# Kernel optimization log

Measured on AMD Instinct MI355X. Metric: run time of the kernel, lower is better.

The kernel has to match this reference:

```python
import jax, jax.numpy as jnp
import numpy as np

B, KEY, D, U, MODES = 16384, 64, 128, 128, 32

def setup_inputs() -> dict:
    key = jax.random.key(0)
    k1, k2, k3, k4, k5 = jax.random.split(key, 5)
    return {
        "key": jax.random.normal(k1, (B, KEY), dtype=jnp.float32),
        "x": jax.random.normal(k2, (B, D), dtype=jnp.float32),
        "sens": jnp.ones((MODES,), dtype=jnp.float32),
        "keys_map": jax.random.normal(k3, (MODES, KEY), dtype=jnp.float32),
        "kernels": jax.random.normal(k4, (MODES, D, U), dtype=jnp.float32) * 0.05,
        "biases": jax.random.normal(k5, (MODES, U), dtype=jnp.float32) * 0.05,
    }

def reference(key, x, sens, keys_map, kernels, biases):
    # key: [B, KEY]; keys_map: [MODES, KEY]
    # Euclidean distance of each key to each mode's stored key.
    dist = jnp.sqrt(jnp.sum((key[:, None, :] - keys_map[None, :, :]) ** 2, axis=-1))  # [B, MODES]
    sim = jax.nn.softmax(sens / (dist + 1.0), axis=-1)  # [B, MODES]
    modes = kernels.shape[0]
    # Original: kernel_b = mean_m(sim[b,m] * kernels[m]); out_b = x_b @ kernel_b.
    # Reordered as GEMM-per-mode + weighted combine (same math):
    out = jnp.einsum('bm,bd,mdu->bu', sim, x, kernels) / modes  # [B, U]
    out = out + (sim @ biases) / modes  # mean over modes of sim-weighted biases
    return out
```

## Files before the change

### kernel.cpp

```cpp
#include <hip/hip_runtime.h>

#define BATCH 16384
#define KEYD  64
#define DDIM  128
#define UDIM  128
#define MODES 32

typedef __attribute__((ext_vector_type(8))) short bf16x8;
typedef __attribute__((ext_vector_type(4))) float f32x4;

__device__ __forceinline__ unsigned short f2bf(float f) {
  unsigned u = __float_as_uint(f);
  unsigned r = (u + 0x7FFFu + ((u >> 16) & 1u)) >> 16;
  return (unsigned short)r;
}

__device__ __forceinline__ void gld_lds16(const void* g, void* l) {
  __builtin_amdgcn_global_load_lds(
      (const __attribute__((address_space(1))) unsigned int*)g,
      (__attribute__((address_space(3))) unsigned int*)l, 16, 0, 0);
}

__global__ __launch_bounds__(256) void prep_all(
    const float* __restrict__ key, const float* __restrict__ x,
    const float* __restrict__ sens, const float* __restrict__ keys_map,
    const float* __restrict__ kernels, const float* __restrict__ biases,
    float* __restrict__ sim, unsigned short* __restrict__ x16,
    unsigned short* __restrict__ kb16, unsigned short* __restrict__ bb16) {
  const int t = threadIdx.x;
  const int bid = blockIdx.x;

  if (bid < BATCH / 32) {
    __shared__ float kr[32][KEYD];
    *(float4*)(&kr[0][0] + t * 4) =
        *(const float4*)(key + (long)bid * 32 * KEYD + t * 4);
    *(float4*)(&kr[0][0] + 1024 + t * 4) =
        *(const float4*)(key + (long)bid * 32 * KEYD + 1024 + t * 4);

    const int lane = t & 63, wave = t >> 6;
    const int m = lane & 31, h = lane >> 5;
    float kreg[32];
    {
      const float* kmp = keys_map + m * KEYD + h * 32;
      #pragma unroll
      for (int j = 0; j < 32; j += 4) {
        const float4 v = *(const float4*)(kmp + j);
        kreg[j] = v.x; kreg[j + 1] = v.y; kreg[j + 2] = v.z; kreg[j + 3] = v.w;
      }
    }
    const float sv = sens[m];
    __syncthreads();

    #pragma unroll
    for (int rr = 0; rr < 8; ++rr) {
      const int rl = wave * 8 + rr;
      const long row = (long)bid * 32 + rl;

      float d2h = 0.f;
      #pragma unroll
      for (int j = 0; j < 32; j += 2) {
        const float2 kv = *(const float2*)(&kr[rl][h * 32 + j]);
        float a = kv.x - kreg[j], b = kv.y - kreg[j + 1];
        d2h += a * a + b * b;
      }
      float d2 = d2h + __shfl_xor(d2h, 32, 64);
      float logit = sv / (sqrtf(d2) + 1.0f);
      float mx = logit;
      #pragma unroll
      for (int off = 16; off > 0; off >>= 1) mx = fmaxf(mx, __shfl_xor(mx, off, 64));
      float e = __expf(logit - mx);
      float s = e;
      #pragma unroll
      for (int off = 16; off > 0; off >>= 1) s += __shfl_xor(s, off, 64);
      if (h == 0) sim[row * MODES + m] = e / s;

      const float2 xv = *(const float2*)(x + row * DDIM + lane * 2);
      ushort2 o; o.x = f2bf(xv.x); o.y = f2bf(xv.y);
      *(ushort2*)(x16 + row * DDIM + lane * 2) = o;
    }
  } else {
    int tt = (bid - BATCH / 32) * 256 + t;
    if (tt < MODES * 16 * UDIM) {
      int u = tt & 127, kb = (tt >> 7) & 15, m = tt >> 11;
      const float* src = kernels + (long)((m * 16 + kb) * 8) * UDIM + u;
      ushort4 lo, hi;
      lo.x = f2bf(src[0 * UDIM]); lo.y = f2bf(src[1 * UDIM]);
      lo.z = f2bf(src[2 * UDIM]); lo.w = f2bf(src[3 * UDIM]);
      hi.x = f2bf(src[4 * UDIM]); hi.y = f2bf(src[5 * UDIM]);
      hi.z = f2bf(src[6 * UDIM]); hi.w = f2bf(src[7 * UDIM]);
      *(ushort4*)(kb16 + (long)tt * 8) = lo;
      *(ushort4*)(kb16 + (long)tt * 8 + 4) = hi;
    } else {
      int tb = tt - MODES * 16 * UDIM;
      int u = tb & 127, kb = tb >> 7;
      const float* src = biases + kb * 8 * UDIM + u;
      ushort4 lo, hi;
      lo.x = f2bf(src[0 * UDIM]); lo.y = f2bf(src[1 * UDIM]);
      lo.z = f2bf(src[2 * UDIM]); lo.w = f2bf(src[3 * UDIM]);
      hi.x = f2bf(src[4 * UDIM]); hi.y = f2bf(src[5 * UDIM]);
      hi.z = f2bf(src[6 * UDIM]); hi.w = f2bf(src[7 * UDIM]);
      *(ushort4*)(bb16 + (long)tb * 8) = lo;
      *(ushort4*)(bb16 + (long)tb * 8 + 4) = hi;
    }
  }
}

#define MODE_STRIDE (16 * UDIM * 8)
#define HALF_STRIDE (16 * 64 * 8)

__global__ __launch_bounds__(256, 2) void gemm_fused(
    const unsigned short* __restrict__ x16, const unsigned short* __restrict__ kb16,
    const unsigned short* __restrict__ bb16, const float* __restrict__ sim,
    float* __restrict__ out) {
  __shared__ alignas(16) unsigned short bsh[2][2 * HALF_STRIDE];
  __shared__ float simT[MODES][64];

  const int t = threadIdx.x;
  const int lane = t & 63, w = t >> 6;
  const int q = lane >> 4, l16 = lane & 15;
  const long bm = (long)blockIdx.x * 64;
  const int ch = blockIdx.y;
  const int uc = w * 16 + l16;

  {
    const int r = t >> 2, mg = (t & 3) * 8;
    const float4 v0 = *(const float4*)(sim + (bm + r) * MODES + mg);
    const float4 v1 = *(const float4*)(sim + (bm + r) * MODES + mg + 4);
    simT[mg + 0][r] = v0.x; simT[mg + 1][r] = v0.y;
    simT[mg + 2][r] = v0.z; simT[mg + 3][r] = v0.w;
    simT[mg + 4][r] = v1.x; simT[mg + 5][r] = v1.y;
    simT[mg + 6][r] = v1.z; simT[mg + 7][r] = v1.w;
  }

  bf16x8 aF[4][4];
  #pragma unroll
  for (int rt = 0; rt < 4; ++rt)
    #pragma unroll
    for (int ks = 0; ks < 4; ++ks)
      aF[rt][ks] = *(const bf16x8*)(x16 + (bm + rt * 16 + l16) * DDIM + ks * 32 + q * 8);

  #pragma unroll
  for (int i = 0; i < 8; ++i) {
    const int c = i * 4 + w, ml = c >> 4, kb = c & 15;
    gld_lds16(kb16 + (long)ml * MODE_STRIDE + kb * (UDIM * 8) + ch * (64 * 8) + lane * 8,
              &bsh[0][(c * 64 + lane) * 8]);
  }

  f32x4 acc[4] = {};

  for (int s = 0; s < MODES / 2; ++s) {
    __syncthreads();
    if (s < MODES / 2 - 1) {
      const unsigned short* srcb = kb16 + (long)(s + 1) * 2 * MODE_STRIDE;
      unsigned short* dst = bsh[(s + 1) & 1];
      #pragma unroll
      for (int i = 0; i < 8; ++i) {
        const int c = i * 4 + w, ml = c >> 4, kb = c & 15;
        gld_lds16(srcb + (long)ml * MODE_STRIDE + kb * (UDIM * 8) + ch * (64 * 8) + lane * 8,
                  dst + (c * 64 + lane) * 8);
      }
    }

    const unsigned short* bs = bsh[s & 1];
    #pragma unroll
    for (int ml = 0; ml < 2; ++ml) {
      const int mi = s * 2 + ml;
      bf16x8 bF[4];
      #pragma unroll
      for (int ks = 0; ks < 4; ++ks)
        bF[ks] = *(const bf16x8*)&bs[ml * HALF_STRIDE + (((ks * 4 + q) * 64) + uc) * 8];

      f32x4 tmp[4] = {};
      #pragma unroll
      for (int ks = 0; ks < 4; ++ks)
        #pragma unroll
        for (int rt = 0; rt < 4; ++rt)
          tmp[rt] = __builtin_amdgcn_mfma_f32_16x16x32_bf16(aF[rt][ks], bF[ks], tmp[rt], 0, 0, 0);

      #pragma unroll
      for (int rt = 0; rt < 4; ++rt) {
        const f32x4 sv = *(const f32x4*)&simT[mi][rt * 16 + q * 4];
        acc[rt] += sv * tmp[rt];
      }
    }
  }

  {
    const bf16x8 bb = *(const bf16x8*)(bb16 + ((long)q * UDIM + ch * 64 + uc) * 8);
    #pragma unroll
    for (int rt = 0; rt < 4; ++rt) {
      const float* sp = sim + (bm + rt * 16 + l16) * MODES + q * 8;
      const float4 sv0 = *(const float4*)(sp);
      const float4 sv1 = *(const float4*)(sp + 4);
      bf16x8 sF;
      sF[0] = (short)f2bf(sv0.x); sF[1] = (short)f2bf(sv0.y);
      sF[2] = (short)f2bf(sv0.z); sF[3] = (short)f2bf(sv0.w);
      sF[4] = (short)f2bf(sv1.x); sF[5] = (short)f2bf(sv1.y);
      sF[6] = (short)f2bf(sv1.z); sF[7] = (short)f2bf(sv1.w);
      acc[rt] = __builtin_amdgcn_mfma_f32_16x16x32_bf16(sF, bb, acc[rt], 0, 0, 0);
    }
  }

  #pragma unroll
  for (int rt = 0; rt < 4; ++rt) {
    const long row = bm + rt * 16 + q * 4;
    #pragma unroll
    for (int r = 0; r < 4; ++r)
      out[(row + r) * UDIM + ch * 64 + uc] = acc[rt][r] * (1.0f / MODES);
  }
}

extern "C" void kernel_launch(void* const* d_in, const int* in_sizes, int n_in,
                              void* d_out, int out_size, void* d_ws, size_t ws_size,
                              hipStream_t stream) {
  const float* key      = (const float*)d_in[0];
  const float* x        = (const float*)d_in[1];
  const float* sens     = (const float*)d_in[2];
  const float* keys_map = (const float*)d_in[3];
  const float* kernels  = (const float*)d_in[4];
  const float* biases   = (const float*)d_in[5];
  float* out = (float*)d_out;

  char* ws = (char*)d_ws;
  float*          sim  = (float*)ws;
  unsigned short* x16  = (unsigned short*)(ws + (2u << 20));
  unsigned short* kb16 = (unsigned short*)(ws + (6u << 20));
  unsigned short* bb16 = (unsigned short*)(ws + (7u << 20));

  prep_all<<<BATCH / 32 + 258, 256, 0, stream>>>(
      key, x, sens, keys_map, kernels, biases, sim, x16, kb16, bb16);
  gemm_fused<<<dim3(BATCH / 64, 2), 256, 0, stream>>>(x16, kb16, bb16, sim, out);
}
```

Measured before the change: 107.9 us.

## Use per-wave private LDS staging with 4-deep vmcnt pipeline and remapped grid

```diff
diff --git a/kernel.cpp b/kernel.cpp
--- a/kernel.cpp
+++ b/kernel.cpp
@@ -106,20 +106,24 @@
 }
 
 #define MODE_STRIDE (16 * UDIM * 8)
-#define HALF_STRIDE (16 * 64 * 8)
+
+#define WAITV(n) asm volatile("s_waitcnt vmcnt(" #n ")" ::: "memory")
 
 __global__ __launch_bounds__(256, 2) void gemm_fused(
     const unsigned short* __restrict__ x16, const unsigned short* __restrict__ kb16,
     const unsigned short* __restrict__ bb16, const float* __restrict__ sim,
     float* __restrict__ out) {
-  __shared__ alignas(16) unsigned short bsh[2][2 * HALF_STRIDE];
+  __shared__ alignas(16) unsigned short bsh[4][4][2048];
   __shared__ float simT[MODES][64];
 
   const int t = threadIdx.x;
   const int lane = t & 63, w = t >> 6;
   const int q = lane >> 4, l16 = lane & 15;
-  const long bm = (long)blockIdx.x * 64;
-  const int ch = blockIdx.y;
+
+  const int bid0 = blockIdx.x;
+  const int lgc = (bid0 & 7) * 64 + (bid0 >> 3);
+  const int bx = lgc >> 1, ch = lgc & 1;
+  const long bm = (long)bx * 64;
   const int uc = w * 16 + l16;
 
   {
@@ -131,6 +135,7 @@
     simT[mg + 4][r] = v1.x; simT[mg + 5][r] = v1.y;
     simT[mg + 6][r] = v1.z; simT[mg + 7][r] = v1.w;
   }
+  __syncthreads();
 
   bf16x8 aF[4][4];
   #pragma unroll
@@ -139,51 +144,47 @@
     for (int ks = 0; ks < 4; ++ks)
       aF[rt][ks] = *(const bf16x8*)(x16 + (bm + rt * 16 + l16) * DDIM + ks * 32 + q * 8);
 
+  const int stg_g = ((lane >> 4) * UDIM + ch * 64 + w * 16 + (lane & 15)) * 8;
+
+#define STAGE(m, p) do {                                                        \
+    const unsigned short* sg = kb16 + (long)(m) * MODE_STRIDE + stg_g;          \
+    _Pragma("unroll")                                                           \
+    for (int j = 0; j < 4; ++j)                                                 \
+      gld_lds16(sg + j * (4 * UDIM * 8), &bsh[w][p][(j * 64 + lane) * 8]);      \
+  } while (0)
+
+  STAGE(0, 0); STAGE(1, 1); STAGE(2, 2);
+
+  f32x4 acc[4] = {};
+
   #pragma unroll
-  for (int i = 0; i < 8; ++i) {
-    const int c = i * 4 + w, ml = c >> 4, kb = c & 15;
-    gld_lds16(kb16 + (long)ml * MODE_STRIDE + kb * (UDIM * 8) + ch * (64 * 8) + lane * 8,
-              &bsh[0][(c * 64 + lane) * 8]);
-  }
-
-  f32x4 acc[4] = {};
-
-  for (int s = 0; s < MODES / 2; ++s) {
-    __syncthreads();
-    if (s < MODES / 2 - 1) {
-      const unsigned short* srcb = kb16 + (long)(s + 1) * 2 * MODE_STRIDE;
-      unsigned short* dst = bsh[(s + 1) & 1];
-      #pragma unroll
-      for (int i = 0; i < 8; ++i) {
-        const int c = i * 4 + w, ml = c >> 4, kb = c & 15;
-        gld_lds16(srcb + (long)ml * MODE_STRIDE + kb * (UDIM * 8) + ch * (64 * 8) + lane * 8,
-                  dst + (c * 64 + lane) * 8);
-      }
-    }
-
-    const unsigned short* bs = bsh[s & 1];
-    #pragma unroll
-    for (int ml = 0; ml < 2; ++ml) {
-      const int mi = s * 2 + ml;
-      bf16x8 bF[4];
-      #pragma unroll
-      for (int ks = 0; ks < 4; ++ks)
-        bF[ks] = *(const bf16x8*)&bs[ml * HALF_STRIDE + (((ks * 4 + q) * 64) + uc) * 8];
-
-      f32x4 tmp[4] = {};
-      #pragma unroll
-      for (int ks = 0; ks < 4; ++ks)
-        #pragma unroll
-        for (int rt = 0; rt < 4; ++rt)
-          tmp[rt] = __builtin_amdgcn_mfma_f32_16x16x32_bf16(aF[rt][ks], bF[ks], tmp[rt], 0, 0, 0);
-
-      #pragma unroll
-      for (int rt = 0; rt < 4; ++rt) {
-        const f32x4 sv = *(const f32x4*)&simT[mi][rt * 16 + q * 4];
-        acc[rt] += sv * tmp[rt];
-      }
-    }
-  }
+  for (int mi = 0; mi < MODES; ++mi) {
+    if (mi < 30) WAITV(8);
+    else if (mi == 30) WAITV(4);
+    else WAITV(0);
+
+    if (mi < MODES - 3) STAGE(mi + 3, (mi + 3) & 3);
+
+    const unsigned short* bs = &bsh[w][mi & 3][0];
+    bf16x8 bF[4];
+    #pragma unroll
+    for (int ks = 0; ks < 4; ++ks)
+      bF[ks] = *(const bf16x8*)&bs[((ks * 4 + q) * 16 + l16) * 8];
+
+    f32x4 tmp[4] = {};
+    #pragma unroll
+    for (int ks = 0; ks < 4; ++ks)
+      #pragma unroll
+      for (int rt = 0; rt < 4; ++rt)
+        tmp[rt] = __builtin_amdgcn_mfma_f32_16x16x32_bf16(aF[rt][ks], bF[ks], tmp[rt], 0, 0, 0);
+
+    #pragma unroll
+    for (int rt = 0; rt < 4; ++rt) {
+      const f32x4 sv = *(const f32x4*)&simT[mi][rt * 16 + q * 4];
+      acc[rt] += sv * tmp[rt];
+    }
+  }
+#undef STAGE
 
   {
     const bf16x8 bb = *(const bf16x8*)(bb16 + ((long)q * UDIM + ch * 64 + uc) * 8);
@@ -229,5 +230,5 @@
 
   prep_all<<<BATCH / 32 + 258, 256, 0, stream>>>(
       key, x, sens, keys_map, kernels, biases, sim, x16, kb16, bb16);
-  gemm_fused<<<dim3(BATCH / 64, 2), 256, 0, stream>>>(x16, kb16, bb16, sim, out);
-}
+  gemm_fused<<<dim3(512), 256, 0, stream>>>(x16, kb16, bb16, sim, out);
+}
```

Measured after the change: 259.6 us. 2.41x slower.
